# Performance work log

Hardware: AMD Instinct MI355X
Metric: run time of the kernel (lower is better)

Reference implementation:

```python
import jax, jax.numpy as jnp
import numpy as np

E_DIM = 64
N_EMBED = 1024
N_TOKENS = 262144


def setup_inputs() -> dict:
    key = jax.random.key(0)
    k1, k2 = jax.random.split(key)
    inp = jax.random.normal(k1, (N_TOKENS, E_DIM), dtype=jnp.float32)
    # codebook init mirrors torch uniform_(-1/n_embed, 1/n_embed)
    embed = jax.random.uniform(k2, (E_DIM, N_EMBED), dtype=jnp.float32,
                               minval=-1.0 / N_EMBED, maxval=1.0 / N_EMBED)
    return {"input": inp, "embed": embed}


def reference(input, embed):
    e_dim, n_embed = embed.shape
    flatten = input.reshape(-1, e_dim)  # [N, e_dim]
    dist = (jnp.sum(flatten * flatten, axis=1, keepdims=True)
            - 2.0 * flatten @ embed
            + jnp.sum(embed * embed, axis=0, keepdims=True))
    embed_idxs = jnp.argmin(dist, axis=1)  # matches (-dist).max(1) indices
    embed_idxs = embed_idxs.reshape(input.shape[:-1])
    quantize = jnp.take(embed.T, embed_idxs, axis=0)  # gather codes -> [..., e_dim]
    # straight-through estimator
    quantize_input_grad = input + jax.lax.stop_gradient(quantize - input)
    return (quantize, input, quantize_input_grad, embed_idxs, embed)
```

## Files before the change

### kernel.cpp

```cpp
#include <hip/hip_runtime.h>
#include <hip/hip_bf16.h>
#include <math.h>

#define E_DIM    64
#define N_EMBED  1024
#define N_TOKENS 262144
#define QCAP     65536

typedef __attribute__((ext_vector_type(8)))  short bf16x8;
typedef __attribute__((ext_vector_type(16))) float f32x16;


__device__ __forceinline__ short f2bf_bits(float f) {
    __hip_bfloat16 h = __float2bfloat16(f);
    return *reinterpret_cast<short*>(&h);
}
__device__ __forceinline__ float bfbits2f(short s) {
    __hip_bfloat16 h = *reinterpret_cast<__hip_bfloat16*>(&s);
    return __bfloat162float(h);
}

__device__ __forceinline__ float exact_d(const float* __restrict__ xrow,
                                         const float* __restrict__ emb,
                                         const float* __restrict__ csum,
                                         float a, int j) {
#pragma clang fp contract(off)
    float b = 0.f;
#pragma unroll
    for (int k = 0; k < E_DIM; ++k) b = fmaf(xrow[k], emb[k * N_EMBED + j], b);
    return (a - 2.0f * b) + csum[j];
}

__global__ __launch_bounds__(256) void vq_csum_kernel(const float* __restrict__ emb,
                                                      float* __restrict__ c_out) {
#pragma clang fp contract(off)
    const int j = blockIdx.x * 256 + threadIdx.x;
    if (j >= N_EMBED) return;
    float e = emb[j];
    float s = e * e;
    for (int k = 1; k < E_DIM; ++k) {
        float ek = emb[k * N_EMBED + j];
        float pk = ek * ek;
        s = s + pk;
    }
    c_out[j] = s;
}

__global__ __launch_bounds__(256) void vq_prep_split(const float* __restrict__ emb,
                                                     short* __restrict__ ehiT,
                                                     short* __restrict__ eloT) {
    const int t = blockIdx.x * 256 + threadIdx.x;
    const int k = t >> 10, n = t & 1023;
    float e = emb[t];
    short hb = f2bf_bits(e);
    float hf = bfbits2f(hb);
    short lb = f2bf_bits(e - hf);
    ehiT[n * E_DIM + k] = hb;
    eloT[n * E_DIM + k] = lb;
}

__device__ __forceinline__ bool lexless(float av, int ai, float bv, int bi) {
    return (av < bv) || (av == bv && ai < bi);
}

__device__ __forceinline__ void tile_epilogue(
    const f32x16& acc, const float* __restrict__ cvp16, int codebase_global,
    int h, float a_tok, float& v1, float& v2, float& v3, int& i1, int& i2) {
#pragma clang fp contract(off)
#pragma unroll
    for (int r = 0; r < 16; ++r) {
        const int row = (r & 3) + 8 * (r >> 2) + 4 * h;
        const float d = fmaf(-2.0f, acc[r], a_tok) + cvp16[r];
        const int idx = codebase_global + row;
        if (d < v3) {
            if (d < v1)      { v3 = v2; v2 = v1; i2 = i1; v1 = d; i1 = idx; }
            else if (d < v2) { v3 = v2; v2 = d;  i2 = idx; }
            else             { v3 = d; }
        }
    }
}

__global__ __launch_bounds__(256, 4) void vq_screen_kernel(
    const float* __restrict__ in, const float* __restrict__ emb,
    const float* __restrict__ csum,
    const short* __restrict__ ehiT, const short* __restrict__ eloT,
    float* __restrict__ out_idx, unsigned int* __restrict__ qcnt,
    unsigned int* __restrict__ queue) {
#pragma clang fp contract(off)
    __shared__ uint4 lds_hi[8 * 128];
    __shared__ uint4 lds_lo[8 * 128];
    __shared__ __align__(16) float lds_c[128];

    const int t = threadIdx.x;
    const int wave = t >> 6;
    const int l = t & 63;
    const int col = l & 31;
    const int h = l >> 5;
    const int tok = blockIdx.x * 128 + wave * 32 + col;
    const float* xrow = in + (size_t)tok * E_DIM;

    float xv[4][8];
#pragma unroll
    for (int s = 0; s < 4; ++s) {
        const float4 u0 = *reinterpret_cast<const float4*>(xrow + s * 16 + h * 8);
        const float4 u1 = *reinterpret_cast<const float4*>(xrow + s * 16 + h * 8 + 4);
        xv[s][0] = u0.x; xv[s][1] = u0.y; xv[s][2] = u0.z; xv[s][3] = u0.w;
        xv[s][4] = u1.x; xv[s][5] = u1.y; xv[s][6] = u1.z; xv[s][7] = u1.w;
    }
    bf16x8 bhi[4], blo[4];
#pragma unroll
    for (int s = 0; s < 4; ++s) {
#pragma unroll
        for (int j = 0; j < 8; ++j) {
            const float x = xv[s][j];
            const short hb = f2bf_bits(x);
            const float hf = bfbits2f(hb);
            const short lb = f2bf_bits(x - hf);
            bhi[s][j] = hb;
            blo[s][j] = lb;
        }
    }

    float sv[8];
#pragma unroll
    for (int j = 0; j < 8; ++j) {
        const float p0 = xv[0][j] * xv[0][j];
        const float p1 = xv[1][j] * xv[1][j];
        const float p2 = xv[2][j] * xv[2][j];
        const float p3 = xv[3][j] * xv[3][j];
        sv[j] = (p0 + p1) + (p2 + p3);
    }
    float hh[8];
#pragma unroll
    for (int j = 0; j < 8; ++j) hh[j] = sv[j] + __shfl_xor(sv[j], 32, 64);
    const float u0 = hh[0] + hh[4], u1 = hh[1] + hh[5];
    const float u2 = hh[2] + hh[6], u3 = hh[3] + hh[7];
    const float a_tok = (u0 + u2) + (u1 + u3);

    float sax_h = 0.f;
#pragma unroll
    for (int s = 0; s < 4; ++s)
#pragma unroll
        for (int j = 0; j < 8; ++j) sax_h += fabsf(xv[s][j]);
    const float sax = sax_h + __shfl_xor(sax_h, 32, 64);

    float v1 = 3.4e38f, v2 = 3.4e38f, v3 = 3.4e38f;
    int i1 = 0, i2 = 0;

    for (int cbase = 0; cbase < N_EMBED; cbase += 128) {
        __syncthreads();
        {
            const int code = t & 127;
            const short* src = (t < 128 ? ehiT : eloT) + (size_t)(cbase + code) * E_DIM;
            uint4* dst = (t < 128 ? lds_hi : lds_lo);
            const uint4* s4 = reinterpret_cast<const uint4*>(src);
#pragma unroll
            for (int j = 0; j < 8; ++j) dst[j * 128 + code] = s4[j];
            if (t < 128) lds_c[t] = csum[cbase + t];
        }
        __syncthreads();

#pragma unroll
        for (int tp = 0; tp < 2; ++tp) {
            const int c0 = tp * 64 + col;
            f32x16 accA, accB;
#pragma unroll
            for (int r = 0; r < 16; ++r) { accA[r] = 0.f; accB[r] = 0.f; }
#pragma unroll
            for (int s = 0; s < 4; ++s) {
                const int slot = 2 * s + h;
                const bf16x8 ahA = *reinterpret_cast<const bf16x8*>(&lds_hi[slot * 128 + c0]);
                const bf16x8 alA = *reinterpret_cast<const bf16x8*>(&lds_lo[slot * 128 + c0]);
                const bf16x8 ahB = *reinterpret_cast<const bf16x8*>(&lds_hi[slot * 128 + c0 + 32]);
                const bf16x8 alB = *reinterpret_cast<const bf16x8*>(&lds_lo[slot * 128 + c0 + 32]);
                accA = __builtin_amdgcn_mfma_f32_32x32x16_bf16(ahA, bhi[s], accA, 0, 0, 0);
                accB = __builtin_amdgcn_mfma_f32_32x32x16_bf16(ahB, bhi[s], accB, 0, 0, 0);
                accA = __builtin_amdgcn_mfma_f32_32x32x16_bf16(ahA, blo[s], accA, 0, 0, 0);
                accB = __builtin_amdgcn_mfma_f32_32x32x16_bf16(ahB, blo[s], accB, 0, 0, 0);
                accA = __builtin_amdgcn_mfma_f32_32x32x16_bf16(alA, bhi[s], accA, 0, 0, 0);
                accB = __builtin_amdgcn_mfma_f32_32x32x16_bf16(alB, bhi[s], accB, 0, 0, 0);
            }
            float cvp[16];
#pragma unroll
            for (int g = 0; g < 4; ++g) {
                const float4 cv = *reinterpret_cast<const float4*>(&lds_c[tp * 64 + 8 * g + 4 * h]);
                cvp[g * 4 + 0] = cv.x; cvp[g * 4 + 1] = cv.y;
                cvp[g * 4 + 2] = cv.z; cvp[g * 4 + 3] = cv.w;
            }
            tile_epilogue(accA, cvp, cbase + tp * 64, h, a_tok, v1, v2, v3, i1, i2);
            float cvp2[16];
#pragma unroll
            for (int g = 0; g < 4; ++g) {
                const float4 cv = *reinterpret_cast<const float4*>(&lds_c[tp * 64 + 32 + 8 * g + 4 * h]);
                cvp2[g * 4 + 0] = cv.x; cvp2[g * 4 + 1] = cv.y;
                cvp2[g * 4 + 2] = cv.z; cvp2[g * 4 + 3] = cv.w;
            }
            tile_epilogue(accB, cvp2, cbase + tp * 64 + 32, h, a_tok, v1, v2, v3, i1, i2);
        }
    }

    const float w1 = __shfl_xor(v1, 32, 64), w2 = __shfl_xor(v2, 32, 64), w3 = __shfl_xor(v3, 32, 64);
    const int   j1 = __shfl_xor(i1, 32, 64), j2 = __shfl_xor(i2, 32, 64);
    const bool bfirst = lexless(w1, j1, v1, i1);
    const float r1v = bfirst ? w1 : v1;  const int r1i = bfirst ? j1 : i1;
    const float cav = bfirst ? v1 : v2;  const int cai = bfirst ? i1 : i2;
    const float cbv = bfirst ? w2 : w1;  const int cbi = bfirst ? j2 : j1;
    const bool bsec = lexless(cbv, cbi, cav, cai);
    const float r2v = bsec ? cbv : cav;  const int r2i = bsec ? cbi : cai;
    const float r3v = bsec ? fminf(cav, bfirst ? w3 : w2)
                           : fminf(cbv, bfirst ? v2 : v3);

    if (l < 32) {
        const float THR = 4e-7f * sax + 8e-7f * fabsf(r1v) + 4e-6f;
        int fin;
        if (r2v > r1v + THR) {
            fin = r1i;
        } else if (r3v > r1v + THR) {
            const float d1 = exact_d(xrow, emb, csum, a_tok, r1i);
            const float d2 = exact_d(xrow, emb, csum, a_tok, r2i);
            fin = (d2 < d1) ? r2i : (d1 < d2) ? r1i : (r1i < r2i ? r1i : r2i);
        } else {
            const unsigned int q = atomicAdd(qcnt, 1u);
            if (q < QCAP) queue[q] = (unsigned int)tok;
            fin = r1i;
        }
        out_idx[tok] = (float)fin;
    }
}

__global__ __launch_bounds__(256) void vq_fallback_kernel(
    const float* __restrict__ in, const float* __restrict__ emb,
    const float* __restrict__ csum, const unsigned int* __restrict__ qcnt,
    const unsigned int* __restrict__ queue, float* __restrict__ out_idx) {
#pragma clang fp contract(off)
    unsigned int nq = *qcnt;
    if (nq > QCAP) nq = QCAP;
    const int l = threadIdx.x & 63;
    for (unsigned int w = blockIdx.x * 4 + (threadIdx.x >> 6); w < nq; w += 512) {
        const int tok = (int)queue[w];
        const float* xrow = in + (size_t)tok * E_DIM;
        float x[E_DIM];
#pragma unroll
        for (int j4 = 0; j4 < 16; ++j4) {
            const float4 u = *reinterpret_cast<const float4*>(xrow + j4 * 4);
            x[j4 * 4 + 0] = u.x; x[j4 * 4 + 1] = u.y;
            x[j4 * 4 + 2] = u.z; x[j4 * 4 + 3] = u.w;
        }
        float s[16];
#pragma unroll
        for (int i = 0; i < 16; ++i)
            s[i] = (x[i] * x[i] + x[i + 16] * x[i + 16]) +
                   (x[i + 32] * x[i + 32] + x[i + 48] * x[i + 48]);
        float hh[8];
#pragma unroll
        for (int i = 0; i < 8; ++i) hh[i] = s[i] + s[i + 8];
        float uu[4];
#pragma unroll
        for (int i = 0; i < 4; ++i) uu[i] = hh[i] + hh[i + 4];
        const float a = (uu[0] + uu[2]) + (uu[1] + uu[3]);

        const int c0 = l * 16;
        float b[16];
#pragma unroll
        for (int q = 0; q < 16; ++q) b[q] = 0.f;
        for (int k = 0; k < E_DIM; ++k) {
            const float xk = x[k];
            const float* er = emb + k * N_EMBED + c0;
#pragma unroll
            for (int q = 0; q < 16; ++q) b[q] = fmaf(xk, er[q], b[q]);
        }
        float bd = 3.4e38f; int bi = 1 << 30;
#pragma unroll
        for (int q = 0; q < 16; ++q) {
            const float d = (a - 2.0f * b[q]) + csum[c0 + q];
            if (d < bd) { bd = d; bi = c0 + q; }
        }
        for (int m = 1; m < 64; m <<= 1) {
            const float od = __shfl_xor(bd, m, 64);
            const int oi = __shfl_xor(bi, m, 64);
            if (od < bd || (od == bd && oi < bi)) { bd = od; bi = oi; }
        }
        if (l == 0) out_idx[tok] = (float)bi;
    }
}

__global__ __launch_bounds__(256) void vq_gather_kernel(
    const float* __restrict__ in, const float* __restrict__ emb,
    const float* __restrict__ idxf,
    float* __restrict__ out_q, float* __restrict__ out_in, float* __restrict__ out_g) {
#pragma clang fp contract(off)
    const size_t j = (size_t)blockIdx.x * 256 + threadIdx.x;
    const int m  = (int)(j >> 4);
    const int k0 = ((int)j & 15) * 4;
    const int idx = (int)idxf[m];

    const float4 x = reinterpret_cast<const float4*>(in)[j];
    const float q0 = emb[(size_t)(k0 + 0) * N_EMBED + idx];
    const float q1 = emb[(size_t)(k0 + 1) * N_EMBED + idx];
    const float q2 = emb[(size_t)(k0 + 2) * N_EMBED + idx];
    const float q3 = emb[(size_t)(k0 + 3) * N_EMBED + idx];

    float4 q = make_float4(q0, q1, q2, q3);
    float4 g;
    g.x = x.x + (q0 - x.x);
    g.y = x.y + (q1 - x.y);
    g.z = x.z + (q2 - x.z);
    g.w = x.w + (q3 - x.w);

    reinterpret_cast<float4*>(out_q)[j]  = q;
    reinterpret_cast<float4*>(out_in)[j] = x;
    reinterpret_cast<float4*>(out_g)[j]  = g;
}

__global__ __launch_bounds__(256) void vq_copy_embed(
    const float* __restrict__ emb, float* __restrict__ out_e) {
    const int i = blockIdx.x * 256 + threadIdx.x;
    reinterpret_cast<float4*>(out_e)[i] = reinterpret_cast<const float4*>(emb)[i];
}

extern "C" void kernel_launch(void* const* d_in, const int* in_sizes, int n_in,
                              void* d_out, int out_size, void* d_ws, size_t ws_size,
                              hipStream_t stream) {
    const float* in  = (const float*)d_in[0];
    const float* emb = (const float*)d_in[1];

    float* out     = (float*)d_out;
    float* out_q   = out;
    float* out_in  = out + (size_t)N_TOKENS * E_DIM;
    float* out_g   = out + 2ull * N_TOKENS * E_DIM;
    float* out_idx = out + 3ull * N_TOKENS * E_DIM;
    float* out_e   = out_idx + N_TOKENS;

    unsigned char* ws = (unsigned char*)d_ws;
    float* c_ws          = (float*)(ws);
    short* ehiT          = (short*)(ws + 4096);
    short* eloT          = (short*)(ws + 4096 + 131072);
    unsigned int* qcnt   = (unsigned int*)(ws + 4096 + 262144);
    unsigned int* queue  = (unsigned int*)(ws + 4096 + 262144 + 64);

    hipMemsetAsync(qcnt, 0, sizeof(unsigned int), stream);

    vq_csum_kernel<<<(N_EMBED + 255) / 256, 256, 0, stream>>>(emb, c_ws);
    vq_prep_split<<<(E_DIM * N_EMBED) / 256, 256, 0, stream>>>(emb, ehiT, eloT);

    vq_screen_kernel<<<N_TOKENS / 128, 256, 0, stream>>>(
        in, emb, c_ws, ehiT, eloT, out_idx, qcnt, queue);

    vq_fallback_kernel<<<128, 256, 0, stream>>>(in, emb, c_ws, qcnt, queue, out_idx);

    const int gather_blocks = (N_TOKENS * E_DIM / 4) / 256;
    vq_gather_kernel<<<gather_blocks, 256, 0, stream>>>(in, emb, out_idx,
                                                        out_q, out_in, out_g);

    vq_copy_embed<<<(E_DIM * N_EMBED / 4) / 256, 256, 0, stream>>>(emb, out_e);
}
```

Measured before the change: 317.6 us.

## Fold distance bias into MFMA and use packed integer top-2 keys in screening

The screening kernel now processes two tokens per lane group, reusing each codebook LDS fragment across twice as many MFMAs. The -2 scale is folded into the precomputed codebook split, and the per-code norm plus an offset constant are added through an extra MFMA against a ones vector. The float epilogue with branches becomes branchless min/second-min tracking on keys that pack the float bits and the code index into one integer. The inline exact two-candidate recheck is removed, and ambiguous or out-of-range tokens are sent to the fallback queue instead. The embed copy is merged into the prep kernel. The risks are more register pressure (occupancy hint lowered from 4 to 2), bf16 rounding of the code norms, and a possibly larger fallback queue.

```diff
diff --git a/kernel.cpp b/kernel.cpp
--- a/kernel.cpp
+++ b/kernel.cpp
@@ -16,23 +16,13 @@
     return *reinterpret_cast<short*>(&h);
 }
 __device__ __forceinline__ float bfbits2f(short s) {
-    __hip_bfloat16 h = *reinterpret_cast<__hip_bfloat16*>(&s);
-    return __bfloat162float(h);
-}
-
-__device__ __forceinline__ float exact_d(const float* __restrict__ xrow,
-                                         const float* __restrict__ emb,
-                                         const float* __restrict__ csum,
-                                         float a, int j) {
-#pragma clang fp contract(off)
-    float b = 0.f;
-#pragma unroll
-    for (int k = 0; k < E_DIM; ++k) b = fmaf(xrow[k], emb[k * N_EMBED + j], b);
-    return (a - 2.0f * b) + csum[j];
+    unsigned int u = ((unsigned int)(unsigned short)s) << 16;
+    return __uint_as_float(u);
 }
 
 __global__ __launch_bounds__(256) void vq_csum_kernel(const float* __restrict__ emb,
-                                                      float* __restrict__ c_out) {
+                                                      float* __restrict__ c_out,
+                                                      unsigned short* __restrict__ cbf) {
 #pragma clang fp contract(off)
     const int j = blockIdx.x * 256 + threadIdx.x;
     if (j >= N_EMBED) return;
@@ -44,188 +34,206 @@
         s = s + pk;
     }
     c_out[j] = s;
+    cbf[j] = (unsigned short)f2bf_bits(s);
 }
 
 __global__ __launch_bounds__(256) void vq_prep_split(const float* __restrict__ emb,
                                                      short* __restrict__ ehiT,
-                                                     short* __restrict__ eloT) {
+                                                     short* __restrict__ eloT,
+                                                     float* __restrict__ out_e) {
     const int t = blockIdx.x * 256 + threadIdx.x;
     const int k = t >> 10, n = t & 1023;
     float e = emb[t];
-    short hb = f2bf_bits(e);
+    float m2 = -2.0f * e;
+    short hb = f2bf_bits(m2);
     float hf = bfbits2f(hb);
-    short lb = f2bf_bits(e - hf);
+    short lb = f2bf_bits(m2 - hf);
     ehiT[n * E_DIM + k] = hb;
     eloT[n * E_DIM + k] = lb;
-}
-
-__device__ __forceinline__ bool lexless(float av, int ai, float bv, int bi) {
-    return (av < bv) || (av == bv && ai < bi);
-}
-
-__device__ __forceinline__ void tile_epilogue(
-    const f32x16& acc, const float* __restrict__ cvp16, int codebase_global,
-    int h, float a_tok, float& v1, float& v2, float& v3, int& i1, int& i2) {
-#pragma clang fp contract(off)
-#pragma unroll
-    for (int r = 0; r < 16; ++r) {
-        const int row = (r & 3) + 8 * (r >> 2) + 4 * h;
-        const float d = fmaf(-2.0f, acc[r], a_tok) + cvp16[r];
-        const int idx = codebase_global + row;
-        if (d < v3) {
-            if (d < v1)      { v3 = v2; v2 = v1; i2 = i1; v1 = d; i1 = idx; }
-            else if (d < v2) { v3 = v2; v2 = d;  i2 = idx; }
-            else             { v3 = d; }
-        }
-    }
-}
-
-__global__ __launch_bounds__(256, 4) void vq_screen_kernel(
-    const float* __restrict__ in, const float* __restrict__ emb,
-    const float* __restrict__ csum,
+    out_e[t] = e;
+}
+
+__global__ __launch_bounds__(256, 2) void vq_screen_kernel(
+    const float* __restrict__ in,
     const short* __restrict__ ehiT, const short* __restrict__ eloT,
-    float* __restrict__ out_idx, unsigned int* __restrict__ qcnt,
-    unsigned int* __restrict__ queue) {
-#pragma clang fp contract(off)
+    const unsigned short* __restrict__ cbf,
+    float* __restrict__ out_idx,
+    unsigned int* __restrict__ qcnt, unsigned int* __restrict__ queue)
+{
     __shared__ uint4 lds_hi[8 * 128];
     __shared__ uint4 lds_lo[8 * 128];
-    __shared__ __align__(16) float lds_c[128];
+    __shared__ unsigned short lds_cb[128];
 
     const int t = threadIdx.x;
-    const int wave = t >> 6;
-    const int l = t & 63;
-    const int col = l & 31;
-    const int h = l >> 5;
-    const int tok = blockIdx.x * 128 + wave * 32 + col;
-    const float* xrow = in + (size_t)tok * E_DIM;
-
-    float xv[4][8];
-#pragma unroll
-    for (int s = 0; s < 4; ++s) {
-        const float4 u0 = *reinterpret_cast<const float4*>(xrow + s * 16 + h * 8);
-        const float4 u1 = *reinterpret_cast<const float4*>(xrow + s * 16 + h * 8 + 4);
-        xv[s][0] = u0.x; xv[s][1] = u0.y; xv[s][2] = u0.z; xv[s][3] = u0.w;
-        xv[s][4] = u1.x; xv[s][5] = u1.y; xv[s][6] = u1.z; xv[s][7] = u1.w;
-    }
-    bf16x8 bhi[4], blo[4];
-#pragma unroll
-    for (int s = 0; s < 4; ++s) {
-#pragma unroll
-        for (int j = 0; j < 8; ++j) {
-            const float x = xv[s][j];
-            const short hb = f2bf_bits(x);
-            const float hf = bfbits2f(hb);
-            const short lb = f2bf_bits(x - hf);
-            bhi[s][j] = hb;
-            blo[s][j] = lb;
-        }
-    }
-
-    float sv[8];
-#pragma unroll
-    for (int j = 0; j < 8; ++j) {
-        const float p0 = xv[0][j] * xv[0][j];
-        const float p1 = xv[1][j] * xv[1][j];
-        const float p2 = xv[2][j] * xv[2][j];
-        const float p3 = xv[3][j] * xv[3][j];
-        sv[j] = (p0 + p1) + (p2 + p3);
-    }
-    float hh[8];
-#pragma unroll
-    for (int j = 0; j < 8; ++j) hh[j] = sv[j] + __shfl_xor(sv[j], 32, 64);
-    const float u0 = hh[0] + hh[4], u1 = hh[1] + hh[5];
-    const float u2 = hh[2] + hh[6], u3 = hh[3] + hh[7];
-    const float a_tok = (u0 + u2) + (u1 + u3);
-
-    float sax_h = 0.f;
-#pragma unroll
-    for (int s = 0; s < 4; ++s)
-#pragma unroll
-        for (int j = 0; j < 8; ++j) sax_h += fabsf(xv[s][j]);
-    const float sax = sax_h + __shfl_xor(sax_h, 32, 64);
-
-    float v1 = 3.4e38f, v2 = 3.4e38f, v3 = 3.4e38f;
-    int i1 = 0, i2 = 0;
-
-    for (int cbase = 0; cbase < N_EMBED; cbase += 128) {
+    const int wave = t >> 6, l = t & 63, col = l & 31, h = l >> 5;
+    const int base = blockIdx.x * 256 + wave * 64;
+    const int tok0 = base + col, tok1 = base + 32 + col;
+
+    bf16x8 bhi0[4], blo0[4], bhi1[4], blo1[4];
+    float sax0h = 0.f, sax1h = 0.f, a0h = 0.f, a1h = 0.f;
+    {
+        const float* xr = in + (size_t)tok0 * E_DIM;
+#pragma unroll
+        for (int s = 0; s < 4; ++s) {
+            float4 u0 = *reinterpret_cast<const float4*>(xr + s * 16 + h * 8);
+            float4 u1 = *reinterpret_cast<const float4*>(xr + s * 16 + h * 8 + 4);
+            float xs[8] = {u0.x, u0.y, u0.z, u0.w, u1.x, u1.y, u1.z, u1.w};
+#pragma unroll
+            for (int j = 0; j < 8; ++j) {
+                float x = xs[j];
+                sax0h += fabsf(x);
+                a0h = fmaf(x, x, a0h);
+                short hb = f2bf_bits(x);
+                bhi0[s][j] = hb;
+                blo0[s][j] = f2bf_bits(x - bfbits2f(hb));
+            }
+        }
+    }
+    {
+        const float* xr = in + (size_t)tok1 * E_DIM;
+#pragma unroll
+        for (int s = 0; s < 4; ++s) {
+            float4 u0 = *reinterpret_cast<const float4*>(xr + s * 16 + h * 8);
+            float4 u1 = *reinterpret_cast<const float4*>(xr + s * 16 + h * 8 + 4);
+            float xs[8] = {u0.x, u0.y, u0.z, u0.w, u1.x, u1.y, u1.z, u1.w};
+#pragma unroll
+            for (int j = 0; j < 8; ++j) {
+                float x = xs[j];
+                sax1h += fabsf(x);
+                a1h = fmaf(x, x, a1h);
+                short hb = f2bf_bits(x);
+                bhi1[s][j] = hb;
+                blo1[s][j] = f2bf_bits(x - bfbits2f(hb));
+            }
+        }
+    }
+
+    bf16x8 ones;
+#pragma unroll
+    for (int j = 0; j < 8; ++j) ones[j] = 0;
+    if (h == 0) { ones[0] = (short)0x3F80; ones[1] = (short)0x3F80; }
+
+    unsigned int g1m0 = 0xFFFFFFFFu, g1c0 = 1023u, g2m0 = 0xFFFFFFFFu;
+    unsigned int g1m1 = 0xFFFFFFFFu, g1c1 = 1023u, g2m1 = 0xFFFFFFFFu;
+
+    for (int cb = 0; cb < N_EMBED; cb += 128) {
         __syncthreads();
         {
             const int code = t & 127;
-            const short* src = (t < 128 ? ehiT : eloT) + (size_t)(cbase + code) * E_DIM;
-            uint4* dst = (t < 128 ? lds_hi : lds_lo);
+            const short* src = ((t < 128) ? ehiT : eloT) + (size_t)(cb + code) * E_DIM;
+            uint4* dst = (t < 128) ? lds_hi : lds_lo;
             const uint4* s4 = reinterpret_cast<const uint4*>(src);
 #pragma unroll
             for (int j = 0; j < 8; ++j) dst[j * 128 + code] = s4[j];
-            if (t < 128) lds_c[t] = csum[cbase + t];
+            if (t < 128) lds_cb[code] = cbf[cb + code];
         }
         __syncthreads();
+
+        unsigned int k10 = 0xFFFFFFFFu, k20 = 0xFFFFFFFFu;
+        unsigned int k11 = 0xFFFFFFFFu, k21 = 0xFFFFFFFFu;
 
 #pragma unroll
         for (int tp = 0; tp < 2; ++tp) {
             const int c0 = tp * 64 + col;
-            f32x16 accA, accB;
-#pragma unroll
-            for (int r = 0; r < 16; ++r) { accA[r] = 0.f; accB[r] = 0.f; }
+            f32x16 aA0, aA1, aB0, aB1;
+#pragma unroll
+            for (int r = 0; r < 16; ++r) { aA0[r] = 0.f; aA1[r] = 0.f; aB0[r] = 0.f; aB1[r] = 0.f; }
 #pragma unroll
             for (int s = 0; s < 4; ++s) {
                 const int slot = 2 * s + h;
-                const bf16x8 ahA = *reinterpret_cast<const bf16x8*>(&lds_hi[slot * 128 + c0]);
-                const bf16x8 alA = *reinterpret_cast<const bf16x8*>(&lds_lo[slot * 128 + c0]);
-                const bf16x8 ahB = *reinterpret_cast<const bf16x8*>(&lds_hi[slot * 128 + c0 + 32]);
-                const bf16x8 alB = *reinterpret_cast<const bf16x8*>(&lds_lo[slot * 128 + c0 + 32]);
-                accA = __builtin_amdgcn_mfma_f32_32x32x16_bf16(ahA, bhi[s], accA, 0, 0, 0);
-                accB = __builtin_amdgcn_mfma_f32_32x32x16_bf16(ahB, bhi[s], accB, 0, 0, 0);
-                accA = __builtin_amdgcn_mfma_f32_32x32x16_bf16(ahA, blo[s], accA, 0, 0, 0);
-                accB = __builtin_amdgcn_mfma_f32_32x32x16_bf16(ahB, blo[s], accB, 0, 0, 0);
-                accA = __builtin_amdgcn_mfma_f32_32x32x16_bf16(alA, bhi[s], accA, 0, 0, 0);
-                accB = __builtin_amdgcn_mfma_f32_32x32x16_bf16(alB, bhi[s], accB, 0, 0, 0);
+                bf16x8 ahA = *reinterpret_cast<const bf16x8*>(&lds_hi[slot * 128 + c0]);
+                bf16x8 alA = *reinterpret_cast<const bf16x8*>(&lds_lo[slot * 128 + c0]);
+                bf16x8 ahB = *reinterpret_cast<const bf16x8*>(&lds_hi[slot * 128 + c0 + 32]);
+                bf16x8 alB = *reinterpret_cast<const bf16x8*>(&lds_lo[slot * 128 + c0 + 32]);
+                aA0 = __builtin_amdgcn_mfma_f32_32x32x16_bf16(ahA, bhi0[s], aA0, 0, 0, 0);
+                aA0 = __builtin_amdgcn_mfma_f32_32x32x16_bf16(ahA, blo0[s], aA0, 0, 0, 0);
+                aA0 = __builtin_amdgcn_mfma_f32_32x32x16_bf16(alA, bhi0[s], aA0, 0, 0, 0);
+                aA1 = __builtin_amdgcn_mfma_f32_32x32x16_bf16(ahA, bhi1[s], aA1, 0, 0, 0);
+                aA1 = __builtin_amdgcn_mfma_f32_32x32x16_bf16(ahA, blo1[s], aA1, 0, 0, 0);
+                aA1 = __builtin_amdgcn_mfma_f32_32x32x16_bf16(alA, bhi1[s], aA1, 0, 0, 0);
+                aB0 = __builtin_amdgcn_mfma_f32_32x32x16_bf16(ahB, bhi0[s], aB0, 0, 0, 0);
+                aB0 = __builtin_amdgcn_mfma_f32_32x32x16_bf16(ahB, blo0[s], aB0, 0, 0, 0);
+                aB0 = __builtin_amdgcn_mfma_f32_32x32x16_bf16(alB, bhi0[s], aB0, 0, 0, 0);
+                aB1 = __builtin_amdgcn_mfma_f32_32x32x16_bf16(ahB, bhi1[s], aB1, 0, 0, 0);
+                aB1 = __builtin_amdgcn_mfma_f32_32x32x16_bf16(ahB, blo1[s], aB1, 0, 0, 0);
+                aB1 = __builtin_amdgcn_mfma_f32_32x32x16_bf16(alB, bhi1[s], aB1, 0, 0, 0);
             }
-            float cvp[16];
-#pragma unroll
-            for (int g = 0; g < 4; ++g) {
-                const float4 cv = *reinterpret_cast<const float4*>(&lds_c[tp * 64 + 8 * g + 4 * h]);
-                cvp[g * 4 + 0] = cv.x; cvp[g * 4 + 1] = cv.y;
-                cvp[g * 4 + 2] = cv.z; cvp[g * 4 + 3] = cv.w;
+            bf16x8 cfA, cfB;
+#pragma unroll
+            for (int j = 0; j < 8; ++j) { cfA[j] = 0; cfB[j] = 0; }
+            cfA[0] = (short)0x4040; cfA[1] = (short)lds_cb[c0];
+            cfB[0] = (short)0x4040; cfB[1] = (short)lds_cb[c0 + 32];
+            aA0 = __builtin_amdgcn_mfma_f32_32x32x16_bf16(cfA, ones, aA0, 0, 0, 0);
+            aA1 = __builtin_amdgcn_mfma_f32_32x32x16_bf16(cfA, ones, aA1, 0, 0, 0);
+            aB0 = __builtin_amdgcn_mfma_f32_32x32x16_bf16(cfB, ones, aB0, 0, 0, 0);
+            aB1 = __builtin_amdgcn_mfma_f32_32x32x16_bf16(cfB, ones, aB1, 0, 0, 0);
+
+            const int rbase = tp * 64 + 4 * h;
+#pragma unroll
+            for (int r = 0; r < 16; ++r) {
+                const unsigned int rcA = (unsigned int)(rbase + (r & 3) + 8 * (r >> 2));
+                const unsigned int rcB = rcA + 32u;
+                unsigned int key, mx;
+                key = (__float_as_uint(aA0[r]) << 7) + rcA;
+                mx = key > k10 ? key : k10; k10 = key < k10 ? key : k10; k20 = mx < k20 ? mx : k20;
+                key = (__float_as_uint(aB0[r]) << 7) + rcB;
+                mx = key > k10 ? key : k10; k10 = key < k10 ? key : k10; k20 = mx < k20 ? mx : k20;
+                key = (__float_as_uint(aA1[r]) << 7) + rcA;
+                mx = key > k11 ? key : k11; k11 = key < k11 ? key : k11; k21 = mx < k21 ? mx : k21;
+                key = (__float_as_uint(aB1[r]) << 7) + rcB;
+                mx = key > k11 ? key : k11; k11 = key < k11 ? key : k11; k21 = mx < k21 ? mx : k21;
             }
-            tile_epilogue(accA, cvp, cbase + tp * 64, h, a_tok, v1, v2, v3, i1, i2);
-            float cvp2[16];
-#pragma unroll
-            for (int g = 0; g < 4; ++g) {
-                const float4 cv = *reinterpret_cast<const float4*>(&lds_c[tp * 64 + 32 + 8 * g + 4 * h]);
-                cvp2[g * 4 + 0] = cv.x; cvp2[g * 4 + 1] = cv.y;
-                cvp2[g * 4 + 2] = cv.z; cvp2[g * 4 + 3] = cv.w;
-            }
-            tile_epilogue(accB, cvp2, cbase + tp * 64 + 32, h, a_tok, v1, v2, v3, i1, i2);
-        }
-    }
-
-    const float w1 = __shfl_xor(v1, 32, 64), w2 = __shfl_xor(v2, 32, 64), w3 = __shfl_xor(v3, 32, 64);
-    const int   j1 = __shfl_xor(i1, 32, 64), j2 = __shfl_xor(i2, 32, 64);
-    const bool bfirst = lexless(w1, j1, v1, i1);
-    const float r1v = bfirst ? w1 : v1;  const int r1i = bfirst ? j1 : i1;
-    const float cav = bfirst ? v1 : v2;  const int cai = bfirst ? i1 : i2;
-    const float cbv = bfirst ? w2 : w1;  const int cbi = bfirst ? j2 : j1;
-    const bool bsec = lexless(cbv, cbi, cav, cai);
-    const float r2v = bsec ? cbv : cav;  const int r2i = bsec ? cbi : cai;
-    const float r3v = bsec ? fminf(cav, bfirst ? w3 : w2)
-                           : fminf(cbv, bfirst ? v2 : v3);
-
-    if (l < 32) {
-        const float THR = 4e-7f * sax + 8e-7f * fabsf(r1v) + 4e-6f;
-        int fin;
-        if (r2v > r1v + THR) {
-            fin = r1i;
-        } else if (r3v > r1v + THR) {
-            const float d1 = exact_d(xrow, emb, csum, a_tok, r1i);
-            const float d2 = exact_d(xrow, emb, csum, a_tok, r2i);
-            fin = (d2 < d1) ? r2i : (d1 < d2) ? r1i : (r1i < r2i ? r1i : r2i);
-        } else {
-            const unsigned int q = atomicAdd(qcnt, 1u);
-            if (q < QCAP) queue[q] = (unsigned int)tok;
-            fin = r1i;
-        }
-        out_idx[tok] = (float)fin;
-    }
+        }
+
+        {
+            unsigned int cm = k10 >> 7, cc = (k10 & 127u) + (unsigned int)cb, c2 = k20 >> 7;
+            unsigned int hi1 = cm > g1m0 ? cm : g1m0;
+            unsigned int lo2 = c2 < g2m0 ? c2 : g2m0;
+            g2m0 = hi1 < lo2 ? hi1 : lo2;
+            if (cm < g1m0 || (cm == g1m0 && cc < g1c0)) { g1m0 = cm; g1c0 = cc; }
+        }
+        {
+            unsigned int cm = k11 >> 7, cc = (k11 & 127u) + (unsigned int)cb, c2 = k21 >> 7;
+            unsigned int hi1 = cm > g1m1 ? cm : g1m1;
+            unsigned int lo2 = c2 < g2m1 ? c2 : g2m1;
+            g2m1 = hi1 < lo2 ? hi1 : lo2;
+            if (cm < g1m1 || (cm == g1m1 && cc < g1c1)) { g1m1 = cm; g1c1 = cc; }
+        }
+    }
+
+    const unsigned int o1m0 = __shfl_xor(g1m0, 32, 64);
+    const unsigned int o1c0 = __shfl_xor(g1c0, 32, 64);
+    const unsigned int o2m0 = __shfl_xor(g2m0, 32, 64);
+    const unsigned int o1m1 = __shfl_xor(g1m1, 32, 64);
+    const unsigned int o1c1 = __shfl_xor(g1c1, 32, 64);
+    const unsigned int o2m1 = __shfl_xor(g2m1, 32, 64);
+    const float sax0 = sax0h + __shfl_xor(sax0h, 32, 64);
+    const float sax1 = sax1h + __shfl_xor(sax1h, 32, 64);
+    const float aa0  = a0h + __shfl_xor(a0h, 32, 64);
+    const float aa1  = a1h + __shfl_xor(a1h, 32, 64);
+
+    const unsigned int a1m = h ? g1m1 : g1m0, a1c = h ? g1c1 : g1c0, a2m = h ? g2m1 : g2m0;
+    const unsigned int b1m = h ? o1m1 : o1m0, b1c = h ? o1c1 : o1c0, b2m = h ? o2m1 : o2m0;
+    const float sx = h ? sax1 : sax0;
+    const float ax = h ? aa1 : aa0;
+    const int tok = h ? tok1 : tok0;
+
+    const unsigned int hi1 = a1m > b1m ? a1m : b1m;
+    const unsigned int lo2 = a2m < b2m ? a2m : b2m;
+    const unsigned int m2 = hi1 < lo2 ? hi1 : lo2;
+    const bool bl = (b1m < a1m) || (b1m == a1m && b1c < a1c);
+    const unsigned int m1 = bl ? b1m : a1m;
+    const unsigned int c1 = bl ? b1c : a1c;
+
+    const float s1 = __uint_as_float(0x40000000u + m1);
+    const float s2 = __uint_as_float(0x40000000u + m2);
+    const float thr = 3e-6f + 2.5e-7f * sx + 5e-7f * ax;
+    const bool q = (s2 - s1 <= thr) || (sx >= 400.f) || (s1 < 2.5f) || (s1 > 3.5f);
+    if (q) {
+        unsigned int qi = atomicAdd(qcnt, 1u);
+        if (qi < QCAP) queue[qi] = (unsigned int)tok;
+    }
+    out_idx[tok] = (float)c1;
 }
 
 __global__ __launch_bounds__(256) void vq_fallback_kernel(
@@ -312,12 +320,6 @@
     reinterpret_cast<float4*>(out_g)[j]  = g;
 }
 
-__global__ __launch_bounds__(256) void vq_copy_embed(
-    const float* __restrict__ emb, float* __restrict__ out_e) {
-    const int i = blockIdx.x * 256 + threadIdx.x;
-    reinterpret_cast<float4*>(out_e)[i] = reinterpret_cast<const float4*>(emb)[i];
-}
-
 extern "C" void kernel_launch(void* const* d_in, const int* in_sizes, int n_in,
                               void* d_out, int out_size, void* d_ws, size_t ws_size,
                               hipStream_t stream) {
@@ -332,25 +334,24 @@
     float* out_e   = out_idx + N_TOKENS;
 
     unsigned char* ws = (unsigned char*)d_ws;
-    float* c_ws          = (float*)(ws);
-    short* ehiT          = (short*)(ws + 4096);
-    short* eloT          = (short*)(ws + 4096 + 131072);
-    unsigned int* qcnt   = (unsigned int*)(ws + 4096 + 262144);
-    unsigned int* queue  = (unsigned int*)(ws + 4096 + 262144 + 64);
+    float*          c_ws  = (float*)(ws);
+    unsigned short* cbf   = (unsigned short*)(ws + 4096);
+    short*          ehiT  = (short*)(ws + 8192);
+    short*          eloT  = (short*)(ws + 8192 + 131072);
+    unsigned int*   qcnt  = (unsigned int*)(ws + 8192 + 262144);
+    unsigned int*   queue = (unsigned int*)(ws + 8192 + 262144 + 64);
 
     hipMemsetAsync(qcnt, 0, sizeof(unsigned int), stream);
 
-    vq_csum_kernel<<<(N_EMBED + 255) / 256, 256, 0, stream>>>(emb, c_ws);
-    vq_prep_split<<<(E_DIM * N_EMBED) / 256, 256, 0, stream>>>(emb, ehiT, eloT);
-
-    vq_screen_kernel<<<N_TOKENS / 128, 256, 0, stream>>>(
-        in, emb, c_ws, ehiT, eloT, out_idx, qcnt, queue);
+    vq_csum_kernel<<<4, 256, 0, stream>>>(emb, c_ws, cbf);
+    vq_prep_split<<<256, 256, 0, stream>>>(emb, ehiT, eloT, out_e);
+
+    vq_screen_kernel<<<N_TOKENS / 256, 256, 0, stream>>>(
+        in, ehiT, eloT, cbf, out_idx, qcnt, queue);
 
     vq_fallback_kernel<<<128, 256, 0, stream>>>(in, emb, c_ws, qcnt, queue, out_idx);
 
     const int gather_blocks = (N_TOKENS * E_DIM / 4) / 256;
     vq_gather_kernel<<<gather_blocks, 256, 0, stream>>>(in, emb, out_idx,
                                                         out_q, out_in, out_g);
-
-    vq_copy_embed<<<(E_DIM * N_EMBED / 4) / 256, 256, 0, stream>>>(emb, out_e);
-}
+}
```

Result: slower. 951.4 us (+199.6%).

## Fuse prep kernels, pre-scale codebook by -2 in chunked layout, drop per-token norm

Applied to the files above, without the earlier changes.

Merges the codebook norm, hi/lo bf16 split and embed copy into one prep kernel. The split codebook is now stored pre-multiplied by -2 in a chunk-contiguous layout, so each screen tile loads into LDS with simple coalesced copies. The screen epilogue no longer adds the token norm and reads code norms from global memory instead of LDS. The fallback queue is halved, fallback gets more blocks, and a sanity gate sends outlier tokens to the exact path. The near-tie threshold changes from relative to absolute, which may change how many tokens need the exact re-check.

```diff
diff --git a/kernel.cpp b/kernel.cpp
--- a/kernel.cpp
+++ b/kernel.cpp
@@ -5,7 +5,7 @@
 #define E_DIM    64
 #define N_EMBED  1024
 #define N_TOKENS 262144
-#define QCAP     65536
+#define FQCAP    32768
 
 typedef __attribute__((ext_vector_type(8)))  short bf16x8;
 typedef __attribute__((ext_vector_type(16))) float f32x16;
@@ -16,8 +16,8 @@
     return *reinterpret_cast<short*>(&h);
 }
 __device__ __forceinline__ float bfbits2f(short s) {
-    __hip_bfloat16 h = *reinterpret_cast<__hip_bfloat16*>(&s);
-    return __bfloat162float(h);
+    unsigned int u = ((unsigned int)(unsigned short)s) << 16;
+    return __uint_as_float(u);
 }
 
 __device__ __forceinline__ float exact_d(const float* __restrict__ xrow,
@@ -31,46 +31,64 @@
     return (a - 2.0f * b) + csum[j];
 }
 
-__global__ __launch_bounds__(256) void vq_csum_kernel(const float* __restrict__ emb,
-                                                      float* __restrict__ c_out) {
-#pragma clang fp contract(off)
-    const int j = blockIdx.x * 256 + threadIdx.x;
-    if (j >= N_EMBED) return;
-    float e = emb[j];
-    float s = e * e;
-    for (int k = 1; k < E_DIM; ++k) {
-        float ek = emb[k * N_EMBED + j];
-        float pk = ek * ek;
-        s = s + pk;
-    }
-    c_out[j] = s;
-}
-
-__global__ __launch_bounds__(256) void vq_prep_split(const float* __restrict__ emb,
-                                                     short* __restrict__ ehiT,
-                                                     short* __restrict__ eloT) {
-    const int t = blockIdx.x * 256 + threadIdx.x;
-    const int k = t >> 10, n = t & 1023;
-    float e = emb[t];
-    short hb = f2bf_bits(e);
-    float hf = bfbits2f(hb);
-    short lb = f2bf_bits(e - hf);
-    ehiT[n * E_DIM + k] = hb;
-    eloT[n * E_DIM + k] = lb;
+__device__ __forceinline__ float a_np_of(const float* x) {
+#pragma clang fp contract(off)
+    float s[16];
+#pragma unroll
+    for (int i = 0; i < 16; ++i)
+        s[i] = (x[i] * x[i] + x[i + 16] * x[i + 16]) +
+               (x[i + 32] * x[i + 32] + x[i + 48] * x[i + 48]);
+    float hh[8];
+#pragma unroll
+    for (int i = 0; i < 8; ++i) hh[i] = s[i] + s[i + 8];
+    float uu[4];
+#pragma unroll
+    for (int i = 0; i < 4; ++i) uu[i] = hh[i] + hh[i + 4];
+    return (uu[0] + uu[2]) + (uu[1] + uu[3]);
 }
 
 __device__ __forceinline__ bool lexless(float av, int ai, float bv, int bi) {
     return (av < bv) || (av == bv && ai < bi);
 }
 
+__global__ __launch_bounds__(256) void vq_prep(const float* __restrict__ emb,
+                                               short* __restrict__ eTc,
+                                               float* __restrict__ out_e,
+                                               float* __restrict__ c_out) {
+    const int b = blockIdx.x;
+    if (b < 256) {
+        const int t = b * 256 + threadIdx.x;
+        const int k = t >> 10, n = t & 1023;
+        float e = emb[t];
+        float m2 = -2.0f * e;
+        short hb = f2bf_bits(m2);
+        short lb = f2bf_bits(m2 - bfbits2f(hb));
+        const int chunk = n >> 7, code = n & 127, slot = k >> 3, jj = k & 7;
+        const int base = chunk * 16384 + (slot * 128 + code) * 8 + jj;
+        eTc[base]        = hb;
+        eTc[base + 8192] = lb;
+        out_e[t] = e;
+    } else {
+#pragma clang fp contract(off)
+        const int j = (b - 256) * 256 + threadIdx.x;
+        float e = emb[j];
+        float s = e * e;
+        for (int k = 1; k < E_DIM; ++k) {
+            float ek = emb[k * N_EMBED + j];
+            float pk = ek * ek;
+            s = s + pk;
+        }
+        c_out[j] = s;
+    }
+}
+
 __device__ __forceinline__ void tile_epilogue(
     const f32x16& acc, const float* __restrict__ cvp16, int codebase_global,
-    int h, float a_tok, float& v1, float& v2, float& v3, int& i1, int& i2) {
-#pragma clang fp contract(off)
+    int h, float& v1, float& v2, float& v3, int& i1, int& i2) {
 #pragma unroll
     for (int r = 0; r < 16; ++r) {
         const int row = (r & 3) + 8 * (r >> 2) + 4 * h;
-        const float d = fmaf(-2.0f, acc[r], a_tok) + cvp16[r];
+        const float d = acc[r] + cvp16[r];
         const int idx = codebase_global + row;
         if (d < v3) {
             if (d < v1)      { v3 = v2; v2 = v1; i2 = i1; v1 = d; i1 = idx; }
@@ -82,84 +100,73 @@
 
 __global__ __launch_bounds__(256, 4) void vq_screen_kernel(
     const float* __restrict__ in, const float* __restrict__ emb,
-    const float* __restrict__ csum,
-    const short* __restrict__ ehiT, const short* __restrict__ eloT,
-    float* __restrict__ out_idx, unsigned int* __restrict__ qcnt,
-    unsigned int* __restrict__ queue) {
-#pragma clang fp contract(off)
-    __shared__ uint4 lds_hi[8 * 128];
-    __shared__ uint4 lds_lo[8 * 128];
-    __shared__ __align__(16) float lds_c[128];
+    const float* __restrict__ csum, const short* __restrict__ eTc,
+    float* __restrict__ out_idx,
+    unsigned int* __restrict__ qcnt, unsigned int* __restrict__ fullQ)
+{
+    __shared__ uint4 lds_e[2048];
 
     const int t = threadIdx.x;
-    const int wave = t >> 6;
-    const int l = t & 63;
-    const int col = l & 31;
-    const int h = l >> 5;
+    const int wave = t >> 6, l = t & 63, col = l & 31, h = l >> 5;
     const int tok = blockIdx.x * 128 + wave * 32 + col;
     const float* xrow = in + (size_t)tok * E_DIM;
 
     float xv[4][8];
 #pragma unroll
     for (int s = 0; s < 4; ++s) {
-        const float4 u0 = *reinterpret_cast<const float4*>(xrow + s * 16 + h * 8);
-        const float4 u1 = *reinterpret_cast<const float4*>(xrow + s * 16 + h * 8 + 4);
+        float4 u0 = *reinterpret_cast<const float4*>(xrow + s * 16 + h * 8);
+        float4 u1 = *reinterpret_cast<const float4*>(xrow + s * 16 + h * 8 + 4);
         xv[s][0] = u0.x; xv[s][1] = u0.y; xv[s][2] = u0.z; xv[s][3] = u0.w;
         xv[s][4] = u1.x; xv[s][5] = u1.y; xv[s][6] = u1.z; xv[s][7] = u1.w;
     }
     bf16x8 bhi[4], blo[4];
+    float sax_h = 0.f;
 #pragma unroll
     for (int s = 0; s < 4; ++s) {
 #pragma unroll
         for (int j = 0; j < 8; ++j) {
-            const float x = xv[s][j];
-            const short hb = f2bf_bits(x);
-            const float hf = bfbits2f(hb);
-            const short lb = f2bf_bits(x - hf);
+            float x = xv[s][j];
+            sax_h += fabsf(x);
+            short hb = f2bf_bits(x);
             bhi[s][j] = hb;
-            blo[s][j] = lb;
-        }
-    }
-
-    float sv[8];
-#pragma unroll
-    for (int j = 0; j < 8; ++j) {
-        const float p0 = xv[0][j] * xv[0][j];
-        const float p1 = xv[1][j] * xv[1][j];
-        const float p2 = xv[2][j] * xv[2][j];
-        const float p3 = xv[3][j] * xv[3][j];
-        sv[j] = (p0 + p1) + (p2 + p3);
-    }
-    float hh[8];
-#pragma unroll
-    for (int j = 0; j < 8; ++j) hh[j] = sv[j] + __shfl_xor(sv[j], 32, 64);
-    const float u0 = hh[0] + hh[4], u1 = hh[1] + hh[5];
-    const float u2 = hh[2] + hh[6], u3 = hh[3] + hh[7];
-    const float a_tok = (u0 + u2) + (u1 + u3);
-
-    float sax_h = 0.f;
-#pragma unroll
-    for (int s = 0; s < 4; ++s)
-#pragma unroll
-        for (int j = 0; j < 8; ++j) sax_h += fabsf(xv[s][j]);
+            blo[s][j] = f2bf_bits(x - bfbits2f(hb));
+        }
+    }
     const float sax = sax_h + __shfl_xor(sax_h, 32, 64);
+
+    float a_np;
+    {
+#pragma clang fp contract(off)
+        float sv[8];
+#pragma unroll
+        for (int j = 0; j < 8; ++j) {
+            float p0 = xv[0][j] * xv[0][j];
+            float p1 = xv[1][j] * xv[1][j];
+            float p2 = xv[2][j] * xv[2][j];
+            float p3 = xv[3][j] * xv[3][j];
+            sv[j] = (p0 + p1) + (p2 + p3);
+        }
+        float hh[8];
+#pragma unroll
+        for (int j = 0; j < 8; ++j) hh[j] = sv[j] + __shfl_xor(sv[j], 32, 64);
+        float u0 = hh[0] + hh[4], u1 = hh[1] + hh[5];
+        float u2 = hh[2] + hh[6], u3 = hh[3] + hh[7];
+        a_np = (u0 + u2) + (u1 + u3);
+    }
 
     float v1 = 3.4e38f, v2 = 3.4e38f, v3 = 3.4e38f;
     int i1 = 0, i2 = 0;
 
-    for (int cbase = 0; cbase < N_EMBED; cbase += 128) {
+    for (int cc = 0; cc < 8; ++cc) {
         __syncthreads();
         {
-            const int code = t & 127;
-            const short* src = (t < 128 ? ehiT : eloT) + (size_t)(cbase + code) * E_DIM;
-            uint4* dst = (t < 128 ? lds_hi : lds_lo);
-            const uint4* s4 = reinterpret_cast<const uint4*>(src);
-#pragma unroll
-            for (int j = 0; j < 8; ++j) dst[j * 128 + code] = s4[j];
-            if (t < 128) lds_c[t] = csum[cbase + t];
+            const uint4* gsrc = reinterpret_cast<const uint4*>(eTc) + cc * 2048;
+#pragma unroll
+            for (int j = 0; j < 8; ++j) lds_e[j * 256 + t] = gsrc[j * 256 + t];
         }
         __syncthreads();
 
+        const int cb = cc << 7;
 #pragma unroll
         for (int tp = 0; tp < 2; ++tp) {
             const int c0 = tp * 64 + col;
@@ -169,10 +176,10 @@
 #pragma unroll
             for (int s = 0; s < 4; ++s) {
                 const int slot = 2 * s + h;
-                const bf16x8 ahA = *reinterpret_cast<const bf16x8*>(&lds_hi[slot * 128 + c0]);
-                const bf16x8 alA = *reinterpret_cast<const bf16x8*>(&lds_lo[slot * 128 + c0]);
-                const bf16x8 ahB = *reinterpret_cast<const bf16x8*>(&lds_hi[slot * 128 + c0 + 32]);
-                const bf16x8 alB = *reinterpret_cast<const bf16x8*>(&lds_lo[slot * 128 + c0 + 32]);
+                bf16x8 ahA = *reinterpret_cast<const bf16x8*>(&lds_e[slot * 128 + c0]);
+                bf16x8 alA = *reinterpret_cast<const bf16x8*>(&lds_e[1024 + slot * 128 + c0]);
+                bf16x8 ahB = *reinterpret_cast<const bf16x8*>(&lds_e[slot * 128 + c0 + 32]);
+                bf16x8 alB = *reinterpret_cast<const bf16x8*>(&lds_e[1024 + slot * 128 + c0 + 32]);
                 accA = __builtin_amdgcn_mfma_f32_32x32x16_bf16(ahA, bhi[s], accA, 0, 0, 0);
                 accB = __builtin_amdgcn_mfma_f32_32x32x16_bf16(ahB, bhi[s], accB, 0, 0, 0);
                 accA = __builtin_amdgcn_mfma_f32_32x32x16_bf16(ahA, blo[s], accA, 0, 0, 0);
@@ -180,22 +187,16 @@
                 accA = __builtin_amdgcn_mfma_f32_32x32x16_bf16(alA, bhi[s], accA, 0, 0, 0);
                 accB = __builtin_amdgcn_mfma_f32_32x32x16_bf16(alB, bhi[s], accB, 0, 0, 0);
             }
-            float cvp[16];
+            float cvpA[16], cvpB[16];
 #pragma unroll
             for (int g = 0; g < 4; ++g) {
-                const float4 cv = *reinterpret_cast<const float4*>(&lds_c[tp * 64 + 8 * g + 4 * h]);
-                cvp[g * 4 + 0] = cv.x; cvp[g * 4 + 1] = cv.y;
-                cvp[g * 4 + 2] = cv.z; cvp[g * 4 + 3] = cv.w;
+                const float4 ca = *reinterpret_cast<const float4*>(&csum[cb + tp * 64 + 8 * g + 4 * h]);
+                const float4 cbv4 = *reinterpret_cast<const float4*>(&csum[cb + tp * 64 + 32 + 8 * g + 4 * h]);
+                cvpA[g*4+0] = ca.x;   cvpA[g*4+1] = ca.y;   cvpA[g*4+2] = ca.z;   cvpA[g*4+3] = ca.w;
+                cvpB[g*4+0] = cbv4.x; cvpB[g*4+1] = cbv4.y; cvpB[g*4+2] = cbv4.z; cvpB[g*4+3] = cbv4.w;
             }
-            tile_epilogue(accA, cvp, cbase + tp * 64, h, a_tok, v1, v2, v3, i1, i2);
-            float cvp2[16];
-#pragma unroll
-            for (int g = 0; g < 4; ++g) {
-                const float4 cv = *reinterpret_cast<const float4*>(&lds_c[tp * 64 + 32 + 8 * g + 4 * h]);
-                cvp2[g * 4 + 0] = cv.x; cvp2[g * 4 + 1] = cv.y;
-                cvp2[g * 4 + 2] = cv.z; cvp2[g * 4 + 3] = cv.w;
-            }
-            tile_epilogue(accB, cvp2, cbase + tp * 64 + 32, h, a_tok, v1, v2, v3, i1, i2);
+            tile_epilogue(accA, cvpA, cb + tp * 64,      h, v1, v2, v3, i1, i2);
+            tile_epilogue(accB, cvpB, cb + tp * 64 + 32, h, v1, v2, v3, i1, i2);
         }
     }
 
@@ -211,33 +212,32 @@
                            : fminf(cbv, bfirst ? v2 : v3);
 
     if (l < 32) {
-        const float THR = 4e-7f * sax + 8e-7f * fabsf(r1v) + 4e-6f;
-        int fin;
-        if (r2v > r1v + THR) {
-            fin = r1i;
-        } else if (r3v > r1v + THR) {
-            const float d1 = exact_d(xrow, emb, csum, a_tok, r1i);
-            const float d2 = exact_d(xrow, emb, csum, a_tok, r2i);
-            fin = (d2 < d1) ? r2i : (d1 < d2) ? r1i : (r1i < r2i ? r1i : r2i);
+        const float thr = 8e-5f + 4e-7f * sax;
+        const bool sane = (a_np < 150.f) && (sax < 128.f) && (fabsf(r1v) < 0.5f);
+        int fin = r1i;
+        if (sane && (r2v - r1v > thr)) {
+        } else if (sane && (r3v - r1v > thr)) {
+            const float d1 = exact_d(xrow, emb, csum, a_np, r1i);
+            const float d2 = exact_d(xrow, emb, csum, a_np, r2i);
+            if (d2 < d1 || (d2 == d1 && r2i < r1i)) fin = r2i;
         } else {
-            const unsigned int q = atomicAdd(qcnt, 1u);
-            if (q < QCAP) queue[q] = (unsigned int)tok;
-            fin = r1i;
+            const unsigned int qi = atomicAdd(qcnt, 1u);
+            if (qi < FQCAP) fullQ[qi] = (unsigned int)tok;
         }
         out_idx[tok] = (float)fin;
     }
 }
 
-__global__ __launch_bounds__(256) void vq_fallback_kernel(
+__global__ __launch_bounds__(256) void vq_full_kernel(
     const float* __restrict__ in, const float* __restrict__ emb,
     const float* __restrict__ csum, const unsigned int* __restrict__ qcnt,
-    const unsigned int* __restrict__ queue, float* __restrict__ out_idx) {
+    const unsigned int* __restrict__ fullQ, float* __restrict__ out_idx) {
 #pragma clang fp contract(off)
     unsigned int nq = *qcnt;
-    if (nq > QCAP) nq = QCAP;
+    if (nq > FQCAP) nq = FQCAP;
     const int l = threadIdx.x & 63;
-    for (unsigned int w = blockIdx.x * 4 + (threadIdx.x >> 6); w < nq; w += 512) {
-        const int tok = (int)queue[w];
+    for (unsigned int w = blockIdx.x * 4 + (threadIdx.x >> 6); w < nq; w += 1024) {
+        const int tok = (int)fullQ[w];
         const float* xrow = in + (size_t)tok * E_DIM;
         float x[E_DIM];
 #pragma unroll
@@ -246,19 +246,7 @@
             x[j4 * 4 + 0] = u.x; x[j4 * 4 + 1] = u.y;
             x[j4 * 4 + 2] = u.z; x[j4 * 4 + 3] = u.w;
         }
-        float s[16];
-#pragma unroll
-        for (int i = 0; i < 16; ++i)
-            s[i] = (x[i] * x[i] + x[i + 16] * x[i + 16]) +
-                   (x[i + 32] * x[i + 32] + x[i + 48] * x[i + 48]);
-        float hh[8];
-#pragma unroll
-        for (int i = 0; i < 8; ++i) hh[i] = s[i] + s[i + 8];
-        float uu[4];
-#pragma unroll
-        for (int i = 0; i < 4; ++i) uu[i] = hh[i] + hh[i + 4];
-        const float a = (uu[0] + uu[2]) + (uu[1] + uu[3]);
-
+        const float a = a_np_of(x);
         const int c0 = l * 16;
         float b[16];
 #pragma unroll
@@ -312,12 +300,6 @@
     reinterpret_cast<float4*>(out_g)[j]  = g;
 }
 
-__global__ __launch_bounds__(256) void vq_copy_embed(
-    const float* __restrict__ emb, float* __restrict__ out_e) {
-    const int i = blockIdx.x * 256 + threadIdx.x;
-    reinterpret_cast<float4*>(out_e)[i] = reinterpret_cast<const float4*>(emb)[i];
-}
-
 extern "C" void kernel_launch(void* const* d_in, const int* in_sizes, int n_in,
                               void* d_out, int out_size, void* d_ws, size_t ws_size,
                               hipStream_t stream) {
@@ -332,25 +314,21 @@
     float* out_e   = out_idx + N_TOKENS;
 
     unsigned char* ws = (unsigned char*)d_ws;
-    float* c_ws          = (float*)(ws);
-    short* ehiT          = (short*)(ws + 4096);
-    short* eloT          = (short*)(ws + 4096 + 131072);
-    unsigned int* qcnt   = (unsigned int*)(ws + 4096 + 262144);
-    unsigned int* queue  = (unsigned int*)(ws + 4096 + 262144 + 64);
+    float*          c_ws  = (float*)(ws);
+    short*          eTc   = (short*)(ws + 4096);
+    unsigned int*   qcnt  = (unsigned int*)(ws + 4096 + 262144);
+    unsigned int*   fullQ = (unsigned int*)(ws + 4096 + 262144 + 256);
 
     hipMemsetAsync(qcnt, 0, sizeof(unsigned int), stream);
 
-    vq_csum_kernel<<<(N_EMBED + 255) / 256, 256, 0, stream>>>(emb, c_ws);
-    vq_prep_split<<<(E_DIM * N_EMBED) / 256, 256, 0, stream>>>(emb, ehiT, eloT);
+    vq_prep<<<260, 256, 0, stream>>>(emb, eTc, out_e, c_ws);
 
     vq_screen_kernel<<<N_TOKENS / 128, 256, 0, stream>>>(
-        in, emb, c_ws, ehiT, eloT, out_idx, qcnt, queue);
-
-    vq_fallback_kernel<<<128, 256, 0, stream>>>(in, emb, c_ws, qcnt, queue, out_idx);
+        in, emb, c_ws, eTc, out_idx, qcnt, fullQ);
+
+    vq_full_kernel<<<256, 256, 0, stream>>>(in, emb, c_ws, qcnt, fullQ, out_idx);
 
     const int gather_blocks = (N_TOKENS * E_DIM / 4) / 256;
     vq_gather_kernel<<<gather_blocks, 256, 0, stream>>>(in, emb, out_idx,
                                                         out_q, out_in, out_g);
-
-    vq_copy_embed<<<(E_DIM * N_EMBED / 4) / 256, 256, 0, stream>>>(emb, out_e);
-}
+}
```

After: 308.5 us. 1.03x faster.
